# Kernel optimization log

Measured on AMD Instinct MI355X. Metric: run time of the kernel, lower is better.

Reference implementation:

```python
import jax, jax.numpy as jnp
import numpy as np

TAU = 2.0      # spikingjelly LIFNode default tau
V_TH = 1.0     # default v_threshold
ALPHA = 4.0    # default surrogate.Sigmoid alpha
H, HL = 8, 2   # num_heads, local_heads

@jax.custom_vjp
def spike(u):
    # Heaviside: fire when membrane potential >= threshold (u = v - v_th)
    return (u >= 0.0).astype(u.dtype)

def _spike_fwd(u):
    return spike(u), u

def _spike_bwd(u, g):
    s = jax.nn.sigmoid(ALPHA * u)
    return (g * ALPHA * s * (1.0 - s),)

spike.defvjp(_spike_fwd, _spike_bwd)

def lif(x):
    # Multi-step LIF, decay_input=False, v_reset=0.0 (hard reset), detach_reset=True.
    # Charge: v = v - (v - 0)/tau + x ; spike when v >= v_th ; reset v -> 0 where spiked.
    decay = 1.0 - 1.0 / TAU
    def step(v, xt):
        v = v * decay + xt
        s = spike(v - V_TH)
        v = v * (1.0 - jax.lax.stop_gradient(s))  # detach_reset
        return v, s
    _, spikes = jax.lax.scan(step, jnp.zeros_like(x[0]), x)
    return spikes

def setup_inputs() -> dict:
    key = jax.random.key(0)
    ks = jax.random.split(key, 5)
    T, B, C, D = 4, 8, 512, 768
    hd = D // H            # 96
    mkv = hd * HL          # 192 (GQA kv projection width)
    scale = 0.1            # keeps LIF membrane potentials near threshold
    return {
        "x": jax.random.normal(ks[0], (T, B, C, D), jnp.float32),
        "q_w": jax.random.normal(ks[1], (D, D), jnp.float32) * scale,
        "k_w": jax.random.normal(ks[2], (mkv, D), jnp.float32) * scale,
        "v_w": jax.random.normal(ks[3], (mkv, D), jnp.float32) * scale,
        "wo_w": jax.random.normal(ks[4], (D, D), jnp.float32) * scale,
    }

def reference(x, q_w, k_w, v_w, wo_w):
    T, B, C, D = x.shape
    hd = D // H
    n_rep = H // HL
    xs = lif(x)  # proj_lif
    # q: (T,B,C,D) -> (T,B,H,C,hd)
    q = lif(xs @ q_w.T).reshape(T, B, C, H, hd).transpose(0, 1, 3, 2, 4)
    # k,v: (T,B,C,mkv) -> repeat_interleave over kv heads -> (T,B,H,C,hd)
    k = lif(xs @ k_w.T).reshape(T, B, C, HL, hd)
    k = jnp.repeat(k, n_rep, axis=3).transpose(0, 1, 3, 2, 4)
    v = lif(xs @ v_w.T).reshape(T, B, C, HL, hd)
    v = jnp.repeat(v, n_rep, axis=3).transpose(0, 1, 3, 2, 4)
    # softmax-free attention: (q k^T) * 0.1 @ v
    scores = jnp.einsum('tbhqd,tbhkd->tbhqk', q, k) * 0.1
    out = jnp.einsum('tbhqk,tbhkd->tbhqd', scores, v)
    # (T,B,H,C,hd) -> (T,B,C,D)
    out = out.transpose(0, 1, 3, 2, 4).reshape(T, B, C, D)
    return out @ wo_w.T
```

## Files before the change

kernel.cpp:

```cpp
#include <hip/hip_runtime.h>

typedef __bf16 bf16;
typedef __bf16 bf16x8 __attribute__((ext_vector_type(8)));
typedef float f32x4 __attribute__((ext_vector_type(4)));

#define T_ 4
#define B_ 8
#define C_ 512
#define D_ 768
#define H_ 8
#define HL_ 2
#define HD_ 96
#define MKV_ 192
#define M2_ 4096
#define BCD_ 3145728
#define M3_ 16384
#define NCOMB 1152
#define SUSP_CAP 65536
#define SUSP_WIN 2e-4f

__device__ __forceinline__ void gld16(const bf16* g, bf16* l) {
    __builtin_amdgcn_global_load_lds(
        (const __attribute__((address_space(1))) unsigned int*)g,
        (__attribute__((address_space(3))) unsigned int*)l, 16, 0, 0);
}

__global__ __launch_bounds__(256) void prep_kernel(
    const float* __restrict__ x, const float* __restrict__ q_w,
    const float* __restrict__ k_w, const float* __restrict__ v_w,
    const float* __restrict__ wo_w, bf16* __restrict__ xs,
    bf16* __restrict__ whi, bf16* __restrict__ wlo, bf16* __restrict__ wo_bf,
    unsigned* __restrict__ susp)
{
    const int t0 = blockIdx.x * 256 + threadIdx.x;
    const int stride = gridDim.x * 256;
    if (t0 == 0) susp[0] = 0;
    for (int i = t0; i < BCD_; i += stride) {
        double v = 0.0;
        #pragma unroll
        for (int t = 0; t < T_; ++t) {
            v = v * 0.5 + (double)x[(size_t)t * BCD_ + i];
            float s = (v >= 1.0) ? 1.0f : 0.0f;
            xs[(size_t)t * BCD_ + i] = (bf16)s;
            if (s != 0.0f) v = 0.0;
        }
    }
    for (int i = t0; i < NCOMB * D_; i += stride) {
        int row = i / D_, col = i - row * D_;
        float v;
        if (row < 768)      v = q_w[(size_t)row * D_ + col];
        else if (row < 960) v = k_w[(size_t)(row - 768) * D_ + col];
        else                v = v_w[(size_t)(row - 960) * D_ + col];
        bf16 h = (bf16)v;
        whi[i] = h;
        wlo[i] = (bf16)(v - (float)h);
    }
    for (int i = t0; i < D_ * D_; i += stride)
        wo_bf[i] = (bf16)wo_w[i];
}

__global__ __launch_bounds__(256) void proj_lif_kernel(
    const bf16* __restrict__ xs, const bf16* __restrict__ Whi,
    const bf16* __restrict__ Wlo,
    bf16* __restrict__ q_sp, bf16* __restrict__ k_sp, bf16* __restrict__ v_sp,
    unsigned* __restrict__ susp)
{
    __shared__ __align__(16) bf16 Alds[T_][64 * 64];
    __shared__ __align__(16) bf16 Hlds[64 * 64];
    __shared__ __align__(16) bf16 Llds[64 * 64];

    const int tid  = threadIdx.x;
    const int wave = tid >> 6, lane = tid & 63;
    const int m16  = lane & 15, quad = lane >> 4;
    const int wm   = wave >> 1, wn = wave & 1;
    const int m0   = blockIdx.x * 64;
    const int n0   = blockIdx.y * 64;

    const int colb = n0 + wn * 32;
    bf16* outp; int Nloc, cb;
    if (colb < 768)      { outp = q_sp; Nloc = 768; cb = colb; }
    else if (colb < 960) { outp = k_sp; Nloc = 192; cb = colb - 768; }
    else                 { outp = v_sp; Nloc = 192; cb = colb - 960; }

    f32x4 acc[T_][2][2];
    #pragma unroll
    for (int t = 0; t < T_; t++)
        #pragma unroll
        for (int a = 0; a < 2; a++)
            #pragma unroll
            for (int b = 0; b < 2; b++) { f32x4 z = {0.f,0.f,0.f,0.f}; acc[t][a][b] = z; }

    for (int k0 = 0; k0 < D_; k0 += 64) {
        __syncthreads();
        #pragma unroll
        for (int j = 0; j < 8; j++) {
            int ci = j * 256 + tid;
            int t = ci >> 9, rem = ci & 511, row = rem >> 3, slot = rem & 7;
            int seg = slot ^ ((row >> 1) & 7);
            gld16(xs + (size_t)(t * M2_ + m0 + row) * D_ + k0 + seg * 8, &Alds[t][rem * 8]);
        }
        #pragma unroll
        for (int j = 0; j < 2; j++) {
            int ci = j * 256 + tid;
            int row = ci >> 3, slot = ci & 7;
            int seg = slot ^ ((row >> 1) & 7);
            gld16(Whi + (size_t)(n0 + row) * D_ + k0 + seg * 8, Hlds + ci * 8);
            gld16(Wlo + (size_t)(n0 + row) * D_ + k0 + seg * 8, Llds + ci * 8);
        }
        __syncthreads();

        #pragma unroll
        for (int kc = 0; kc < 2; kc++) {
            bf16x8 a[T_][2], bh[2], bl[2];
            #pragma unroll
            for (int mi = 0; mi < 2; mi++) {
                int row = wm * 32 + mi * 16 + m16;
                int off = row * 64 + (((kc * 4 + quad) ^ ((row >> 1) & 7)) * 8);
                #pragma unroll
                for (int t = 0; t < T_; t++)
                    a[t][mi] = *(const bf16x8*)&Alds[t][off];
            }
            #pragma unroll
            for (int ni = 0; ni < 2; ni++) {
                int row = wn * 32 + ni * 16 + m16;
                int off = row * 64 + (((kc * 4 + quad) ^ ((row >> 1) & 7)) * 8);
                bh[ni] = *(const bf16x8*)&Hlds[off];
                bl[ni] = *(const bf16x8*)&Llds[off];
            }
            #pragma unroll
            for (int ni = 0; ni < 2; ni++)
                #pragma unroll
                for (int t = 0; t < T_; t++)
                    #pragma unroll
                    for (int mi = 0; mi < 2; mi++) {
                        acc[t][mi][ni] = __builtin_amdgcn_mfma_f32_16x16x32_bf16(a[t][mi], bh[ni], acc[t][mi][ni], 0, 0, 0);
                        acc[t][mi][ni] = __builtin_amdgcn_mfma_f32_16x16x32_bf16(a[t][mi], bl[ni], acc[t][mi][ni], 0, 0, 0);
                    }
        }
    }

    #pragma unroll
    for (int mi = 0; mi < 2; mi++)
        #pragma unroll
        for (int ni = 0; ni < 2; ni++)
            #pragma unroll
            for (int rr = 0; rr < 4; rr++) {
                int row = m0 + wm * 32 + mi * 16 + quad * 4 + rr;
                int lc  = cb + ni * 16 + m16;
                float v = 0.f;
                bool suspect = false;
                #pragma unroll
                for (int t = 0; t < T_; t++) {
                    v = v * 0.5f + acc[t][mi][ni][rr];
                    float d = v - 1.0f;
                    if (fabsf(d) < SUSP_WIN) suspect = true;
                    float sp = (d >= 0.f) ? 1.f : 0.f;
                    v *= (1.f - sp);
                    outp[(size_t)(t * M2_ + row) * Nloc + lc] = (bf16)sp;
                }
                if (suspect) {
                    int ccol = n0 + wn * 32 + ni * 16 + m16;
                    unsigned idx = atomicAdd(susp, 1u);
                    if (idx < SUSP_CAP) susp[1 + idx] = (unsigned)(row * 2048 + ccol);
                }
            }
}

__global__ __launch_bounds__(256) void fixup_kernel(
    const bf16* __restrict__ xs, const float* __restrict__ q_w,
    const float* __restrict__ k_w, const float* __restrict__ v_w,
    bf16* __restrict__ q_sp, bf16* __restrict__ k_sp, bf16* __restrict__ v_sp,
    const unsigned* __restrict__ susp)
{
    unsigned count = susp[0];
    if (count > SUSP_CAP) count = SUSP_CAP;
    const int lane = threadIdx.x & 63;
    const int wid  = (blockIdx.x * blockDim.x + threadIdx.x) >> 6;
    const int nw   = (gridDim.x * blockDim.x) >> 6;
    for (unsigned i = wid; i < count; i += nw) {
        unsigned e = susp[1 + i];
        int row = e >> 11, col = e & 2047;
        const float* W; bf16* outp; int Nloc, lc;
        if (col < 768)      { W = q_w + (size_t)col * D_;         outp = q_sp; Nloc = 768; lc = col; }
        else if (col < 960) { W = k_w + (size_t)(col - 768) * D_; outp = k_sp; Nloc = 192; lc = col - 768; }
        else                { W = v_w + (size_t)(col - 960) * D_; outp = v_sp; Nloc = 192; lc = col - 960; }
        double v = 0.0;
        for (int t = 0; t < T_; ++t) {
            const bf16* ar = xs + (size_t)(t * M2_ + row) * D_;
            double y = 0.0;
            for (int k = lane; k < D_; k += 64)
                y += (double)(float)ar[k] * (double)W[k];
            #pragma unroll
            for (int off = 1; off < 64; off <<= 1)
                y += __shfl_xor(y, off);
            v = v * 0.5 + y;
            unsigned sp = (v >= 1.0) ? 1u : 0u;
            if (lane == 0) outp[(size_t)(t * M2_ + row) * Nloc + lc] = (bf16)(float)sp;
            if (sp) v = 0.0;
        }
    }
}

__global__ __launch_bounds__(256) void ktv_kernel(
    const bf16* __restrict__ k_sp, const bf16* __restrict__ v_sp,
    float* __restrict__ M_part)
{
    const int g    = blockIdx.x;
    const int cc   = blockIdx.y;
    const int kvh  = g % HL_;
    const int tb   = g / HL_;
    const int wave = threadIdx.x >> 6;
    const int lane = threadIdx.x & 63;
    const int m16  = lane & 15, quad = lane >> 4;

    __shared__ __align__(16) bf16 klds[96 * 40];
    __shared__ __align__(16) bf16 vlds[96 * 40];

    f32x4 acc[9];
    #pragma unroll
    for (int i = 0; i < 9; i++) { f32x4 z = {0.f,0.f,0.f,0.f}; acc[i] = z; }

    const bf16* kbase = k_sp + ((size_t)tb * C_ + cc * 128) * MKV_ + kvh * HD_;
    const bf16* vbase = v_sp + ((size_t)tb * C_ + cc * 128) * MKV_ + kvh * HD_;

    for (int c0 = 0; c0 < 128; c0 += 32) {
        __syncthreads();
        for (int idx = threadIdx.x; idx < 32 * 96; idx += 256) {
            int d = idx % 96;
            int c = idx / 96;
            klds[d * 40 + c] = kbase[(size_t)(c0 + c) * MKV_ + d];
            vlds[d * 40 + c] = vbase[(size_t)(c0 + c) * MKV_ + d];
        }
        __syncthreads();
        #pragma unroll
        for (int i = 0; i < 9; i++) {
            int tile = wave + i * 4;
            int mt = tile / 6, nt = tile % 6;
            bf16x8 a = *(const bf16x8*)(&klds[(mt * 16 + m16) * 40 + quad * 8]);
            bf16x8 b = *(const bf16x8*)(&vlds[(nt * 16 + m16) * 40 + quad * 8]);
            acc[i] = __builtin_amdgcn_mfma_f32_16x16x32_bf16(a, b, acc[i], 0, 0, 0);
        }
    }
    float* op = M_part + ((size_t)cc * 64 + g) * HD_ * HD_;
    #pragma unroll
    for (int i = 0; i < 9; i++) {
        int tile = wave + i * 4;
        int mt = tile / 6, nt = tile % 6;
        #pragma unroll
        for (int r = 0; r < 4; r++) {
            int d = mt * 16 + quad * 4 + r;
            int j = nt * 16 + m16;
            op[(size_t)j * HD_ + d] = acc[i][r];
        }
    }
}

__global__ __launch_bounds__(256) void cvtM_kernel(
    const float* __restrict__ M_part, bf16* __restrict__ M_hi,
    bf16* __restrict__ M_lo)
{
    int i = blockIdx.x * 256 + threadIdx.x;
    if (i >= 64 * HD_ * HD_) return;
    float m = M_part[i] + M_part[i + 589824] + M_part[i + 2 * 589824] + M_part[i + 3 * 589824];
    bf16 h = (bf16)m;
    M_hi[i] = h;
    M_lo[i] = (bf16)(m - (float)h);
}

__global__ __launch_bounds__(256) void qm_kernel(
    const bf16* __restrict__ q_sp, const bf16* __restrict__ M_hi,
    const bf16* __restrict__ M_lo, bf16* __restrict__ out_attn)
{
    const int tbh  = blockIdx.x;
    const int h    = tbh % H_;
    const int tb   = tbh / H_;
    const int g    = tb * HL_ + (h >> 2);
    const int wave = threadIdx.x >> 6;
    const int lane = threadIdx.x & 63;
    const int m16  = lane & 15, quad = lane >> 4;
    const int cw   = blockIdx.y * 128 + wave * 32;

    __shared__ __align__(16) bf16 Mh[96 * 104];
    __shared__ __align__(16) bf16 Ml[96 * 104];
    {
        const bf16* gh = M_hi + (size_t)g * HD_ * HD_;
        const bf16* gl = M_lo + (size_t)g * HD_ * HD_;
        #pragma unroll
        for (int j = 0; j < 5; j++) {
            int ci = j * 256 + threadIdx.x;
            if (ci < 1152) {
                int row = ci / 12, seg = ci % 12;
                *(bf16x8*)&Mh[row * 104 + seg * 8] = *(const bf16x8*)(gh + row * HD_ + seg * 8);
                *(bf16x8*)&Ml[row * 104 + seg * 8] = *(const bf16x8*)(gl + row * HD_ + seg * 8);
            }
        }
    }
    __syncthreads();

    f32x4 acc[2][6];
    #pragma unroll
    for (int mi = 0; mi < 2; mi++)
        #pragma unroll
        for (int nt = 0; nt < 6; nt++) { f32x4 z = {0.f,0.f,0.f,0.f}; acc[mi][nt] = z; }

    #pragma unroll
    for (int ks = 0; ks < 3; ++ks) {
        bf16x8 a[2];
        #pragma unroll
        for (int mi = 0; mi < 2; mi++)
            a[mi] = *(const bf16x8*)(q_sp + ((size_t)(tb * C_ + cw + mi * 16 + m16)) * D_
                                     + h * HD_ + ks * 32 + quad * 8);
        #pragma unroll
        for (int nt = 0; nt < 6; ++nt) {
            bf16x8 bh = *(const bf16x8*)&Mh[(nt * 16 + m16) * 104 + ks * 32 + quad * 8];
            bf16x8 bl = *(const bf16x8*)&Ml[(nt * 16 + m16) * 104 + ks * 32 + quad * 8];
            #pragma unroll
            for (int mi = 0; mi < 2; mi++) {
                acc[mi][nt] = __builtin_amdgcn_mfma_f32_16x16x32_bf16(a[mi], bh, acc[mi][nt], 0, 0, 0);
                acc[mi][nt] = __builtin_amdgcn_mfma_f32_16x16x32_bf16(a[mi], bl, acc[mi][nt], 0, 0, 0);
            }
        }
    }
    #pragma unroll
    for (int mi = 0; mi < 2; mi++)
        #pragma unroll
        for (int nt = 0; nt < 6; nt++)
            #pragma unroll
            for (int r = 0; r < 4; r++) {
                int c = cw + mi * 16 + quad * 4 + r;
                int j = nt * 16 + m16;
                out_attn[((size_t)(tb * C_ + c)) * D_ + h * HD_ + j] = (bf16)(0.1f * acc[mi][nt][r]);
            }
}

__global__ __launch_bounds__(256) void final_gemm_kernel(
    const bf16* __restrict__ A, const bf16* __restrict__ W, float* __restrict__ out)
{
    __shared__ __align__(16) bf16 Alds[128 * 64];
    __shared__ __align__(16) bf16 Blds[128 * 64];
    const int tid  = threadIdx.x;
    const int wave = tid >> 6, lane = tid & 63;
    const int m16  = lane & 15, quad = lane >> 4;
    const int wm   = wave >> 1, wn = wave & 1;
    const int m0   = blockIdx.x * 128, n0 = blockIdx.y * 128;

    f32x4 acc[4][4];
    #pragma unroll
    for (int a = 0; a < 4; a++)
        #pragma unroll
        for (int b = 0; b < 4; b++) { f32x4 z = {0.f,0.f,0.f,0.f}; acc[a][b] = z; }

    for (int k0 = 0; k0 < D_; k0 += 64) {
        __syncthreads();
        #pragma unroll
        for (int j = 0; j < 4; j++) {
            int ci = j * 256 + tid;
            int row = ci >> 3, slot = ci & 7;
            int seg = slot ^ ((row >> 1) & 7);
            gld16(A + (size_t)(m0 + row) * D_ + k0 + seg * 8, Alds + ci * 8);
            gld16(W + (size_t)(n0 + row) * D_ + k0 + seg * 8, Blds + ci * 8);
        }
        __syncthreads();
        #pragma unroll
        for (int kc = 0; kc < 2; kc++) {
            bf16x8 a[4], b[4];
            #pragma unroll
            for (int mi = 0; mi < 4; mi++) {
                int row = wm * 64 + mi * 16 + m16;
                a[mi] = *(const bf16x8*)&Alds[row * 64 + (((kc * 4 + quad) ^ ((row >> 1) & 7)) * 8)];
            }
            #pragma unroll
            for (int ni = 0; ni < 4; ni++) {
                int row = wn * 64 + ni * 16 + m16;
                b[ni] = *(const bf16x8*)&Blds[row * 64 + (((kc * 4 + quad) ^ ((row >> 1) & 7)) * 8)];
            }
            #pragma unroll
            for (int mi = 0; mi < 4; mi++)
                #pragma unroll
                for (int ni = 0; ni < 4; ni++)
                    acc[mi][ni] = __builtin_amdgcn_mfma_f32_16x16x32_bf16(a[mi], b[ni], acc[mi][ni], 0, 0, 0);
        }
    }
    #pragma unroll
    for (int mi = 0; mi < 4; mi++)
        #pragma unroll
        for (int ni = 0; ni < 4; ni++)
            #pragma unroll
            for (int r = 0; r < 4; r++) {
                int row = m0 + wm * 64 + mi * 16 + quad * 4 + r;
                int col = n0 + wn * 64 + ni * 16 + m16;
                out[(size_t)row * D_ + col] = acc[mi][ni][r];
            }
}

extern "C" void kernel_launch(void* const* d_in, const int* in_sizes, int n_in,
                              void* d_out, int out_size, void* d_ws, size_t ws_size,
                              hipStream_t stream) {
    const float* x    = (const float*)d_in[0];
    const float* q_w  = (const float*)d_in[1];
    const float* k_w  = (const float*)d_in[2];
    const float* v_w  = (const float*)d_in[3];
    const float* wo_w = (const float*)d_in[4];
    float* out = (float*)d_out;

    char* ws = (char*)d_ws;
    bf16* xs    = (bf16*)(ws);
    bf16* q_sp  = (bf16*)(ws + 25165824);
    bf16* k_sp  = (bf16*)(ws + 50331648);
    bf16* v_sp  = (bf16*)(ws + 56623104);
    bf16* whi   = (bf16*)(ws + 62914560);
    bf16* wlo   = (bf16*)(ws + 64684032);
    bf16* wo_bf = (bf16*)(ws + 66453504);
    bf16* M_hi  = (bf16*)(ws + 67633152);
    bf16* M_lo  = (bf16*)(ws + 68812800);
    unsigned* susp = (unsigned*)(ws + 69992448);
    bf16* out_attn = xs;
    float* M_part  = out;

    hipLaunchKernelGGL(prep_kernel, dim3(2048), dim3(256), 0, stream,
                       x, q_w, k_w, v_w, wo_w, xs, whi, wlo, wo_bf, susp);
    hipLaunchKernelGGL(proj_lif_kernel, dim3(M2_ / 64, NCOMB / 64), dim3(256), 0, stream,
                       xs, whi, wlo, q_sp, k_sp, v_sp, susp);
    hipLaunchKernelGGL(fixup_kernel, dim3(256), dim3(256), 0, stream,
                       xs, q_w, k_w, v_w, q_sp, k_sp, v_sp, susp);
    hipLaunchKernelGGL(ktv_kernel, dim3(T_ * B_ * HL_, 4), dim3(256), 0, stream,
                       k_sp, v_sp, M_part);
    hipLaunchKernelGGL(cvtM_kernel, dim3((64 * HD_ * HD_ + 255) / 256), dim3(256), 0, stream,
                       M_part, M_hi, M_lo);
    hipLaunchKernelGGL(qm_kernel, dim3(T_ * B_ * H_, C_ / 128), dim3(256), 0, stream,
                       q_sp, M_hi, M_lo, out_attn);
    hipLaunchKernelGGL(final_gemm_kernel, dim3(M3_ / 128, D_ / 128), dim3(256), 0, stream,
                       out_attn, wo_bf, out);
}
```

Baseline: 278.8 us.

## Double-buffer projection GEMM, remap blocks per XCD, split K^T V over more chunks

The projection+LIF GEMM now uses a double-buffered LDS pipeline with 32-wide K steps. The next tile's global-to-LDS loads are issued before the current tile's MFMAs, and MFMA priority is raised. Block IDs are remapped so neighbouring M tiles land on the same XCD for L2 reuse, and launch bounds ask for 3 blocks per SM. The K^T V kernel splits the sequence into 8 chunks instead of 4 and loads with 16-byte vectors, so cvtM now sums 8 partials, which adds partial-buffer traffic.

```diff
diff --git a/kernel.cpp b/kernel.cpp
--- a/kernel.cpp
+++ b/kernel.cpp
@@ -59,22 +59,26 @@
         wo_bf[i] = (bf16)wo_w[i];
 }
 
-__global__ __launch_bounds__(256) void proj_lif_kernel(
+__global__ __launch_bounds__(256, 3) void proj_lif_kernel(
     const bf16* __restrict__ xs, const bf16* __restrict__ Whi,
     const bf16* __restrict__ Wlo,
     bf16* __restrict__ q_sp, bf16* __restrict__ k_sp, bf16* __restrict__ v_sp,
     unsigned* __restrict__ susp)
 {
-    __shared__ __align__(16) bf16 Alds[T_][64 * 64];
-    __shared__ __align__(16) bf16 Hlds[64 * 64];
-    __shared__ __align__(16) bf16 Llds[64 * 64];
+    __shared__ __align__(16) bf16 Alds[2][T_][64 * 32];
+    __shared__ __align__(16) bf16 Hlds[2][64 * 32];
+    __shared__ __align__(16) bf16 Llds[2][64 * 32];
 
     const int tid  = threadIdx.x;
     const int wave = tid >> 6, lane = tid & 63;
     const int m16  = lane & 15, quad = lane >> 4;
     const int wm   = wave >> 1, wn = wave & 1;
-    const int m0   = blockIdx.x * 64;
-    const int n0   = blockIdx.y * 64;
+
+    const int bid   = blockIdx.y * 64 + blockIdx.x;
+    const int xcd   = bid & 7;
+    const int local = bid >> 3;
+    const int m0    = ((xcd << 3) | (local & 7)) * 64;
+    const int n0    = (local >> 3) * 64;
 
     const int colb = n0 + wn * 32;
     bf16* outp; int Nloc, cb;
@@ -90,53 +94,56 @@
             #pragma unroll
             for (int b = 0; b < 2; b++) { f32x4 z = {0.f,0.f,0.f,0.f}; acc[t][a][b] = z; }
 
-    for (int k0 = 0; k0 < D_; k0 += 64) {
-        __syncthreads();
-        #pragma unroll
-        for (int j = 0; j < 8; j++) {
-            int ci = j * 256 + tid;
-            int t = ci >> 9, rem = ci & 511, row = rem >> 3, slot = rem & 7;
-            int seg = slot ^ ((row >> 1) & 7);
-            gld16(xs + (size_t)(t * M2_ + m0 + row) * D_ + k0 + seg * 8, &Alds[t][rem * 8]);
-        }
-        #pragma unroll
-        for (int j = 0; j < 2; j++) {
-            int ci = j * 256 + tid;
-            int row = ci >> 3, slot = ci & 7;
-            int seg = slot ^ ((row >> 1) & 7);
-            gld16(Whi + (size_t)(n0 + row) * D_ + k0 + seg * 8, Hlds + ci * 8);
-            gld16(Wlo + (size_t)(n0 + row) * D_ + k0 + seg * 8, Llds + ci * 8);
-        }
-        __syncthreads();
-
-        #pragma unroll
-        for (int kc = 0; kc < 2; kc++) {
-            bf16x8 a[T_][2], bh[2], bl[2];
-            #pragma unroll
-            for (int mi = 0; mi < 2; mi++) {
-                int row = wm * 32 + mi * 16 + m16;
-                int off = row * 64 + (((kc * 4 + quad) ^ ((row >> 1) & 7)) * 8);
+    auto stage = [&](int buf, int k0) {
+        const int row = tid >> 2;
+        const int seg = (tid & 3) ^ ((tid >> 3) & 3);
+        #pragma unroll
+        for (int j = 0; j < T_; j++)
+            gld16(xs + (size_t)(j * M2_ + m0 + row) * D_ + k0 + seg * 8,
+                  &Alds[buf][j][tid * 8]);
+        gld16(Whi + (size_t)(n0 + row) * D_ + k0 + seg * 8, &Hlds[buf][tid * 8]);
+        gld16(Wlo + (size_t)(n0 + row) * D_ + k0 + seg * 8, &Llds[buf][tid * 8]);
+    };
+
+    stage(0, 0);
+    asm volatile("s_waitcnt vmcnt(0)" ::: "memory");
+    __builtin_amdgcn_s_barrier();
+
+    int cur = 0;
+    for (int s = 0; s < 24; ++s) {
+        if (s + 1 < 24) stage(cur ^ 1, (s + 1) * 32);
+
+        bf16x8 a[T_][2], bh[2], bl[2];
+        #pragma unroll
+        for (int mi = 0; mi < 2; mi++) {
+            int row = wm * 32 + mi * 16 + m16;
+            int off = row * 32 + (((quad) ^ ((row >> 1) & 3)) * 8);
+            #pragma unroll
+            for (int t = 0; t < T_; t++)
+                a[t][mi] = *(const bf16x8*)&Alds[cur][t][off];
+        }
+        #pragma unroll
+        for (int ni = 0; ni < 2; ni++) {
+            int row = wn * 32 + ni * 16 + m16;
+            int off = row * 32 + (((quad) ^ ((row >> 1) & 3)) * 8);
+            bh[ni] = *(const bf16x8*)&Hlds[cur][off];
+            bl[ni] = *(const bf16x8*)&Llds[cur][off];
+        }
+        __builtin_amdgcn_s_setprio(1);
+        #pragma unroll
+        for (int ni = 0; ni < 2; ni++)
+            #pragma unroll
+            for (int t = 0; t < T_; t++)
                 #pragma unroll
-                for (int t = 0; t < T_; t++)
-                    a[t][mi] = *(const bf16x8*)&Alds[t][off];
-            }
-            #pragma unroll
-            for (int ni = 0; ni < 2; ni++) {
-                int row = wn * 32 + ni * 16 + m16;
-                int off = row * 64 + (((kc * 4 + quad) ^ ((row >> 1) & 7)) * 8);
-                bh[ni] = *(const bf16x8*)&Hlds[off];
-                bl[ni] = *(const bf16x8*)&Llds[off];
-            }
-            #pragma unroll
-            for (int ni = 0; ni < 2; ni++)
-                #pragma unroll
-                for (int t = 0; t < T_; t++)
-                    #pragma unroll
-                    for (int mi = 0; mi < 2; mi++) {
-                        acc[t][mi][ni] = __builtin_amdgcn_mfma_f32_16x16x32_bf16(a[t][mi], bh[ni], acc[t][mi][ni], 0, 0, 0);
-                        acc[t][mi][ni] = __builtin_amdgcn_mfma_f32_16x16x32_bf16(a[t][mi], bl[ni], acc[t][mi][ni], 0, 0, 0);
-                    }
-        }
+                for (int mi = 0; mi < 2; mi++) {
+                    acc[t][mi][ni] = __builtin_amdgcn_mfma_f32_16x16x32_bf16(a[t][mi], bh[ni], acc[t][mi][ni], 0, 0, 0);
+                    acc[t][mi][ni] = __builtin_amdgcn_mfma_f32_16x16x32_bf16(a[t][mi], bl[ni], acc[t][mi][ni], 0, 0, 0);
+                }
+        __builtin_amdgcn_s_setprio(0);
+
+        asm volatile("s_waitcnt vmcnt(0)" ::: "memory");
+        __builtin_amdgcn_s_barrier();
+        cur ^= 1;
     }
 
     #pragma unroll
@@ -220,16 +227,21 @@
     #pragma unroll
     for (int i = 0; i < 9; i++) { f32x4 z = {0.f,0.f,0.f,0.f}; acc[i] = z; }
 
-    const bf16* kbase = k_sp + ((size_t)tb * C_ + cc * 128) * MKV_ + kvh * HD_;
-    const bf16* vbase = v_sp + ((size_t)tb * C_ + cc * 128) * MKV_ + kvh * HD_;
-
-    for (int c0 = 0; c0 < 128; c0 += 32) {
+    const bf16* kbase = k_sp + ((size_t)tb * C_ + cc * 64) * MKV_ + kvh * HD_;
+    const bf16* vbase = v_sp + ((size_t)tb * C_ + cc * 64) * MKV_ + kvh * HD_;
+
+    for (int c0 = 0; c0 < 64; c0 += 32) {
         __syncthreads();
-        for (int idx = threadIdx.x; idx < 32 * 96; idx += 256) {
-            int d = idx % 96;
-            int c = idx / 96;
-            klds[d * 40 + c] = kbase[(size_t)(c0 + c) * MKV_ + d];
-            vlds[d * 40 + c] = vbase[(size_t)(c0 + c) * MKV_ + d];
+        for (int ci = threadIdx.x; ci < 768; ci += 256) {
+            int arr = ci & 1;
+            int pos = ci >> 1;
+            int c = pos / 12, seg = pos - c * 12;
+            const bf16* src = (arr ? vbase : kbase) + (size_t)(c0 + c) * MKV_ + seg * 8;
+            bf16x8 val = *(const bf16x8*)src;
+            bf16* dst = arr ? vlds : klds;
+            #pragma unroll
+            for (int e = 0; e < 8; e++)
+                dst[(seg * 8 + e) * 40 + c] = val[e];
         }
         __syncthreads();
         #pragma unroll
@@ -261,7 +273,10 @@
 {
     int i = blockIdx.x * 256 + threadIdx.x;
     if (i >= 64 * HD_ * HD_) return;
-    float m = M_part[i] + M_part[i + 589824] + M_part[i + 2 * 589824] + M_part[i + 3 * 589824];
+    float m = 0.f;
+    #pragma unroll
+    for (int j = 0; j < 8; j++)
+        m += M_part[i + (size_t)j * 589824];
     bf16 h = (bf16)m;
     M_hi[i] = h;
     M_lo[i] = (bf16)(m - (float)h);
@@ -423,7 +438,7 @@
                        xs, whi, wlo, q_sp, k_sp, v_sp, susp);
     hipLaunchKernelGGL(fixup_kernel, dim3(256), dim3(256), 0, stream,
                        xs, q_w, k_w, v_w, q_sp, k_sp, v_sp, susp);
-    hipLaunchKernelGGL(ktv_kernel, dim3(T_ * B_ * HL_, 4), dim3(256), 0, stream,
+    hipLaunchKernelGGL(ktv_kernel, dim3(T_ * B_ * HL_, 8), dim3(256), 0, stream,
                        k_sp, v_sp, M_part);
     hipLaunchKernelGGL(cvtM_kernel, dim3((64 * HD_ * HD_ + 255) / 256), dim3(256), 0, stream,
                        M_part, M_hi, M_lo);
```

Measured after the change: 276.9 us. About the same (-0.7%).
